# Optimization experiments

Measured on AMD Instinct MI355X. Metric: run time of the kernel, lower is better.

The kernel has to match this reference:

```python
import jax, jax.numpy as jnp
import numpy as np

B = 256          # batch
C = 1024         # d_in / d_out
S = 14           # spacial_dim
H = 8            # heads
DK = 64          # d_k
DV = 64          # d_v
N = S * S + 1    # tokens incl. mean token (197)
CONV_CH = [8, 32, 64, 128, 256, 1024]
EPS = 1e-5


def setup_inputs() -> dict:
    key = jax.random.key(0)
    ks = iter(jax.random.split(key, 32))
    d = {}
    d['feature_map'] = jax.random.normal(next(ks), (B, C, S, S), jnp.float32)
    d['loss_map'] = jax.random.normal(next(ks), (B, CONV_CH[0], S, S), jnp.float32)
    # 1x1 conv weights stored as (out_ch, in_ch)
    for i in range(5):
        cin, cout = CONV_CH[i], CONV_CH[i + 1]
        d[f'w{i+1}'] = jax.random.normal(next(ks), (cout, cin), jnp.float32) / np.sqrt(cin).astype(np.float32)
        d[f'b{i+1}'] = jnp.zeros((cout,), jnp.float32)
    # attention projections (torch Linear layout: (out, in)), xavier-ish scale
    for name, (o, i_) in [('wq', (H * DK, C)), ('wk', (H * DK, C)), ('wv', (H * DV, C)), ('wo', (C, H * DV))]:
        d[name] = jax.random.normal(next(ks), (o, i_), jnp.float32) * np.sqrt(2.0 / (o + i_)).astype(np.float32)
        d['b' + name[1]] = jnp.zeros((o,), jnp.float32)
    d['ln_g'] = jnp.ones((C,), jnp.float32)
    d['ln_b'] = jnp.zeros((C,), jnp.float32)
    d['pos_kv'] = jax.random.normal(next(ks), (N, C), jnp.float32) / np.sqrt(C).astype(np.float32)
    d['pos_q'] = jax.random.normal(next(ks), (N, C), jnp.float32) / np.sqrt(C).astype(np.float32)
    return d


def _conv1x1(x, w, b):
    # x: (b, cin, h, w); w: (cout, cin)
    return jnp.einsum('bchw,oc->bohw', x, w) + b[None, :, None, None]


def _tokens(m):
    # (b, c, h, w) -> (b, h*w, c) with prepended mean token -> (b, h*w+1, c)
    b = m.shape[0]
    t = m.reshape(b, m.shape[1], -1).transpose(0, 2, 1)
    return jnp.concatenate([t.mean(axis=1, keepdims=True), t], axis=1)


def reference(feature_map, loss_map, w1, b1, w2, b2, w3, b3, w4, b4, w5, b5,
              wq, bq, wk, bk, wv, bv, wo, bo, ln_g, ln_b, pos_kv, pos_q):
    b = feature_map.shape[0]
    # 5-stage 1x1 conv chain (pure linear, no nonlinearity)
    lm = loss_map
    for w, bi in ((w1, b1), (w2, b2), (w3, b3), (w4, b4), (w5, b5)):
        lm = _conv1x1(lm, w, bi)
    x = _tokens(feature_map) + pos_kv[None]        # (b, N, C) keys/values
    lm_t = _tokens(lm) + pos_q[None]               # (b, N, C)
    queries = lm_t[:, :1]                          # (b, 1, C) single query
    # multi-head single-query cross-attention
    q = (queries @ wq.T + bq).reshape(b, 1, H, DK).transpose(0, 2, 1, 3)   # (b,h,1,dk)
    k = (x @ wk.T + bk).reshape(b, N, H, DK).transpose(0, 2, 1, 3)         # (b,h,N,dk)
    v = (x @ wv.T + bv).reshape(b, N, H, DV).transpose(0, 2, 1, 3)         # (b,h,N,dv)
    att = jnp.einsum('bhqd,bhkd->bhqk', q, k) / jnp.asarray(np.sqrt(DK), jnp.float32)
    w_att = jax.nn.softmax(att, axis=-1)
    out = jnp.einsum('bhqk,bhkd->bhqd', w_att, v).transpose(0, 2, 1, 3).reshape(b, 1, H * DV)
    out = out @ wo.T + bo                          # (b, 1, C)
    # residual + layernorm
    res = queries + out
    mu = res.mean(axis=-1, keepdims=True)
    var = ((res - mu) ** 2).mean(axis=-1, keepdims=True)
    out = (res - mu) * jax.lax.rsqrt(var + EPS) * ln_g + ln_b
    return out.squeeze(1)                          # (b, C)
```

## Files before the change

kernel.cpp:

```cpp
#include <hip/hip_runtime.h>

#define WS_WC     ((size_t)0)
#define WS_BCQ    ((size_t)8192)
#define WS_WQP    ((size_t)9216)
#define WS_BQP    ((size_t)13312)
#define WS_U      ((size_t)13824)
#define WS_V      ((size_t)13888)
#define WS_G      ((size_t)14336)
#define WS_G0     ((size_t)79872)
#define WS_POST   ((size_t)88064)
#define WS_PSUM   ((size_t)301056)
#define WS_M0     ((size_t)302080)
#define WS_ATTP   ((size_t)304128)
#define WS_WFM    ((size_t)2008064)
#define WS_WPOS   ((size_t)2434048)
#define WS_S      ((size_t)2860032)
#define WS_OVP    ((size_t)4957184)
#define WS_O1P    ((size_t)6005760)
#define WS_POSTP  ((size_t)7054336)
#define WS_OV     ((size_t)7259136)
#define WS_M4     WS_S
#define WS_PP     WS_OVP

__global__ __launch_bounds__(256) void kp1a_chain_post(
    const float* __restrict__ w1, const float* __restrict__ b1,
    const float* __restrict__ w2, const float* __restrict__ b2,
    const float* __restrict__ w3, const float* __restrict__ b3,
    const float* __restrict__ w4, const float* __restrict__ b4,
    const float* __restrict__ pos_kv, float* __restrict__ ws)
{
  __shared__ float shm[12864];
  const int t = threadIdx.x;
  if (blockIdx.x == 0) {
    float* wt  = shm;
    float* M2s = shm + 8320;
    float* C2s = shm + 8832;
    float* M3s = shm + 8896;
    float* C3s = shm + 9920;
    float* M4s = shm + 10048;
    float* C4s = shm + 12096;

    for (int idx = t; idx < 2048; idx += 256) {
      const float4 v = ((const float4*)w3)[idx];
      const int r = idx >> 4, i = (idx & 15) * 4;
      float* d = &wt[r * 65 + i];
      d[0] = v.x; d[1] = v.y; d[2] = v.z; d[3] = v.w;
    }
    for (int idx = t; idx < 512; idx += 256) {
      const int o = idx >> 3, j = idx & 7;
      float a = 0.f;
      for (int i = 0; i < 32; ++i) a += w2[o*32+i] * w1[i*8+j];
      M2s[idx] = a;
    }
    if (t < 64) {
      float a = b2[t];
      for (int i = 0; i < 32; ++i) a += w2[t*32+i] * b1[i];
      C2s[t] = a;
    }
    __syncthreads();
    for (int idx = t; idx < 1024; idx += 256) {
      const int o = idx >> 3, j = idx & 7;
      const float* wr = &wt[o * 65];
      float a = 0.f;
      for (int i = 0; i < 64; ++i) a += wr[i] * M2s[i*8+j];
      M3s[idx] = a;
    }
    if (t < 128) {
      const float* wr = &wt[t * 65];
      float a = b3[t];
      for (int i = 0; i < 64; ++i) a += wr[i] * C2s[i];
      C3s[t] = a;
    }
    __syncthreads();
    for (int oc = 0; oc < 4; ++oc) {
      for (int idx = t; idx < 2048; idx += 256) {
        const float4 v = ((const float4*)w4)[oc*2048 + idx];
        const int r = idx >> 5, i = (idx & 31) * 4;
        float* d = &wt[r * 129 + i];
        d[0] = v.x; d[1] = v.y; d[2] = v.z; d[3] = v.w;
      }
      __syncthreads();
      for (int idx = t; idx < 512; idx += 256) {
        const int r = idx >> 3, j = idx & 7;
        const float* wr = &wt[r * 129];
        float a = 0.f;
        for (int i = 0; i < 128; ++i) a += wr[i] * M3s[i*8+j];
        M4s[(oc*64 + r)*8 + j] = a;
      }
      if (t < 64) {
        const float* wr = &wt[t * 129];
        float a = b4[oc*64 + t];
        for (int i = 0; i < 128; ++i) a += wr[i] * C3s[i];
        C4s[oc*64 + t] = a;
      }
      __syncthreads();
    }
    for (int idx = t; idx < 2048; idx += 256) ws[WS_M4 + idx] = M4s[idx];
    ws[WS_M4 + 2048 + t] = C4s[t];
  } else {
    const int c0 = (blockIdx.x - 1) * 64;
    const int c = t & 63, nb = t >> 6;
    for (int n = nb; n < 197; n += 4)
      shm[c*201 + n] = pos_kv[(size_t)n*1024 + c0 + c];
    __syncthreads();
    for (int idx = t; idx < 64*208; idx += 256) {
      int cc = idx / 208, n = idx - cc*208;
      ws[WS_POST + (size_t)(c0+cc)*208 + n] = (n < 197) ? shm[cc*201+n] : 0.f;
    }
    for (int idx = t; idx < 64*196; idx += 256) {
      int cc = idx / 196, p = idx - cc*196;
      ws[WS_POSTP + (size_t)(c0+cc)*200 + p] = shm[cc*201 + p + 1];
    }
    if (t < 64) {
      float s = 0.f;
      for (int n = 1; n < 197; ++n) s += shm[t*201 + n];
      ws[WS_PSUM + c0 + t] = s;
    }
  }
}

__global__ __launch_bounds__(256) void kp1b_w5fold(
    const float* __restrict__ w5, const float* __restrict__ b5,
    const float* __restrict__ pos_q, float* __restrict__ ws)
{
  __shared__ float wt[32 * 257];
  __shared__ float M4s[2304];
  const int t = threadIdx.x, ob = blockIdx.x;
  const int o0 = ob * 32;
  for (int idx = t; idx < 2304; idx += 256) M4s[idx] = ws[WS_M4 + idx];
  for (int idx = t; idx < 2048; idx += 256) {
    const float4 v = ((const float4*)w5)[(size_t)ob*2048 + idx];
    const int r = idx >> 6, i = (idx & 63) * 4;
    float* d = &wt[r * 257 + i];
    d[0] = v.x; d[1] = v.y; d[2] = v.z; d[3] = v.w;
  }
  __syncthreads();
  const int r = t >> 3, j = t & 7;
  const float* wr = &wt[r * 257];
  float a = 0.f;
  for (int i = 0; i < 256; ++i) a += wr[i] * M4s[i*8 + j];
  ws[WS_WC + (size_t)(o0 + r)*8 + j] = a;
  if (t < 32) {
    const float* wb = &wt[t * 257];
    float a2 = b5[o0 + t];
    for (int i = 0; i < 256; ++i) a2 += wb[i] * M4s[2048 + i];
    ws[WS_BCQ + o0 + t] = a2 + pos_q[o0 + t];
  }
}

__global__ __launch_bounds__(256) void kp2a_qproj(
    const float* __restrict__ wq, const float* __restrict__ bq,
    float* __restrict__ ws)
{
  const int t = threadIdx.x;
  const int w = t >> 6, l = t & 63;
  const int o = blockIdx.x * 4 + w;
  const float* wqr = wq + (size_t)o * 1024;
  float acc[8] = {0,0,0,0,0,0,0,0};
  float accb = 0.f;
  for (int k = 0; k < 16; ++k) {
    const int c = l + 64*k;
    const float wv_ = wqr[c];
    const float4 a  = *(const float4*)&ws[WS_WC + (size_t)c*8];
    const float4 b2 = *(const float4*)&ws[WS_WC + (size_t)c*8 + 4];
    acc[0] += wv_*a.x;  acc[1] += wv_*a.y;  acc[2] += wv_*a.z;  acc[3] += wv_*a.w;
    acc[4] += wv_*b2.x; acc[5] += wv_*b2.y; acc[6] += wv_*b2.z; acc[7] += wv_*b2.w;
    accb += wv_ * ws[WS_BCQ + c];
  }
  for (int off = 32; off >= 1; off >>= 1) {
#pragma unroll
    for (int j = 0; j < 8; ++j) acc[j] += __shfl_xor(acc[j], off);
    accb += __shfl_xor(accb, off);
  }
  if (l == 0) {
#pragma unroll
    for (int j = 0; j < 8; ++j) ws[WS_WQP + (size_t)o*8 + j] = acc[j];
    ws[WS_BQP + o] = accb + bq[o];
  }
}

__global__ __launch_bounds__(256) void kp2b_gfold(
    const float* __restrict__ wk, const float* __restrict__ bk,
    const float* __restrict__ pos_kv, float* __restrict__ ws)
{
  const int ci = blockIdx.x, h = blockIdx.y, t = threadIdx.x;
  __shared__ float WQs[512];
  __shared__ float BQs[64];
  __shared__ float red2[18 * 256];
  for (int idx = t; idx < 512; idx += 256) WQs[idx] = ws[WS_WQP + (size_t)h*512 + idx];
  if (t < 64) BQs[t] = ws[WS_BQP + h*64 + t];
  __syncthreads();

  const int c = ci*256 + t;
  float accG[8] = {0,0,0,0,0,0,0,0};
  float accg0 = 0.f;
  const float* wkc = wk + (size_t)h*64*1024 + c;
  for (int d = 0; d < 64; ++d) {
    const float wkv = wkc[(size_t)d*1024];
    const float4 qa = *(const float4*)&WQs[d*8];
    const float4 qb = *(const float4*)&WQs[d*8+4];
    accG[0] += wkv*qa.x; accG[1] += wkv*qa.y; accG[2] += wkv*qa.z; accG[3] += wkv*qa.w;
    accG[4] += wkv*qb.x; accG[5] += wkv*qb.y; accG[6] += wkv*qb.z; accG[7] += wkv*qb.w;
    accg0 += wkv * BQs[d];
  }
  *(float4*)&ws[WS_G + ((size_t)h*1024 + c)*8 + 0] = make_float4(accG[0],accG[1],accG[2],accG[3]);
  *(float4*)&ws[WS_G + ((size_t)h*1024 + c)*8 + 4] = make_float4(accG[4],accG[5],accG[6],accG[7]);
  ws[WS_G0 + (size_t)h*1024 + c] = accg0;

  const float z0 = pos_kv[c];
  const float zs = ws[WS_PSUM + c];
#pragma unroll
  for (int j = 0; j < 8; ++j) {
    red2[j*256 + t]     = accG[j]*z0;
    red2[(8+j)*256 + t] = accG[j]*zs;
  }
  red2[16*256 + t] = accg0*z0;
  red2[17*256 + t] = accg0*zs;
  __syncthreads();
  for (int s2 = 128; s2 >= 1; s2 >>= 1) {
    if (t < s2) {
#pragma unroll
      for (int j = 0; j < 18; ++j) red2[j*256 + t] += red2[j*256 + t + s2];
    }
    __syncthreads();
  }
  if (t == 0) {
    float* pp = &ws[WS_PP + ((size_t)ci*8 + h)*18];
#pragma unroll
    for (int j = 0; j < 18; ++j) pp[j] = red2[j*256];
  }

  if (ci == 0) {
    __syncthreads();
    const float bkv = (t < 64) ? bk[h*64 + t] : 0.f;
#pragma unroll
    for (int j = 0; j < 8; ++j)
      red2[j*256 + t] = (t < 64) ? bkv * WQs[t*8 + j] : 0.f;
    red2[8*256 + t] = (t < 64) ? bkv * BQs[t] : 0.f;
    __syncthreads();
    for (int s2 = 128; s2 >= 1; s2 >>= 1) {
      if (t < s2) {
#pragma unroll
        for (int j = 0; j < 9; ++j) red2[j*256 + t] += red2[j*256 + t + s2];
      }
      __syncthreads();
    }
    if (t == 0) {
#pragma unroll
      for (int j = 0; j < 8; ++j) ws[WS_U + h*8 + j] = red2[j*256];
      ws[WS_V + h] = red2[8*256];
    }
  }
}

__global__ __launch_bounds__(256) void ka_att(
    const float* __restrict__ fm, const float* __restrict__ lmap,
    float* __restrict__ ws)
{
  const int ci = blockIdx.x, b = blockIdx.y, t = threadIdx.x;
  __shared__ float qk[256 * 8];
  __shared__ float pa[3 * 49 * 33];
  __shared__ float m0s[8];
  {
    const int ch = t >> 5, lp = t & 31;
    float s = 0.f;
    for (int p = lp; p < 196; p += 32) s += lmap[((size_t)b*8 + ch)*196 + p];
    for (int off = 16; off >= 1; off >>= 1) s += __shfl_xor(s, off);
    if (lp == 0) m0s[ch] = s * (1.f/196.f);
  }
  __syncthreads();
  float m0r[8];
#pragma unroll
  for (int j = 0; j < 8; ++j) m0r[j] = m0s[j];
  const int c0 = ci * 256;
  {
    const int c = c0 + t;
#pragma unroll
    for (int h = 0; h < 8; ++h) {
      const float* gr = &ws[WS_G + ((size_t)h*1024 + c)*8];
      const float4 ga = *(const float4*)gr;
      const float4 gb = *(const float4*)(gr + 4);
      qk[t*8 + h] = ws[WS_G0 + (size_t)h*1024 + c]
                  + ga.x*m0r[0] + ga.y*m0r[1] + ga.z*m0r[2] + ga.w*m0r[3]
                  + gb.x*m0r[4] + gb.y*m0r[5] + gb.z*m0r[6] + gb.w*m0r[7];
    }
  }
  if (ci == 0 && t < 8) ws[WS_M0 + (size_t)b*8 + t] = m0s[t];
  __syncthreads();
  const int q = t >> 6, tl = t & 63;
  float a0[8] = {0,0,0,0,0,0,0,0};
  float a1[8] = {0,0,0,0,0,0,0,0};
  float a2[8] = {0,0,0,0,0,0,0,0};
  float a3[8] = {0,0,0,0,0,0,0,0};
  if (tl < 49) {
    const float* fmp = fm + ((size_t)b*1024 + c0 + q*64)*196 + 4*tl;
    const float* pp  = &ws[WS_POSTP + (size_t)(c0 + q*64)*200 + 4*tl];
    const float* qkh = &qk[q*64*8];
#pragma unroll 2
    for (int cc = 0; cc < 64; ++cc) {
      const float4 f = *(const float4*)&fmp[(size_t)cc*196];
      const float4 g = *(const float4*)&pp[(size_t)cc*200];
      const float x0 = f.x + g.x, x1 = f.y + g.y, x2 = f.z + g.z, x3 = f.w + g.w;
      const float4 qa = *(const float4*)&qkh[cc*8];
      const float4 qb = *(const float4*)&qkh[cc*8 + 4];
      a0[0] += qa.x*x0; a1[0] += qa.x*x1; a2[0] += qa.x*x2; a3[0] += qa.x*x3;
      a0[1] += qa.y*x0; a1[1] += qa.y*x1; a2[1] += qa.y*x2; a3[1] += qa.y*x3;
      a0[2] += qa.z*x0; a1[2] += qa.z*x1; a2[2] += qa.z*x2; a3[2] += qa.z*x3;
      a0[3] += qa.w*x0; a1[3] += qa.w*x1; a2[3] += qa.w*x2; a3[3] += qa.w*x3;
      a0[4] += qb.x*x0; a1[4] += qb.x*x1; a2[4] += qb.x*x2; a3[4] += qb.x*x3;
      a0[5] += qb.y*x0; a1[5] += qb.y*x1; a2[5] += qb.y*x2; a3[5] += qb.y*x3;
      a0[6] += qb.z*x0; a1[6] += qb.z*x1; a2[6] += qb.z*x2; a3[6] += qb.z*x3;
      a0[7] += qb.w*x0; a1[7] += qb.w*x1; a2[7] += qb.w*x2; a3[7] += qb.w*x3;
    }
  }
  if (q > 0 && tl < 49) {
    float* d = &pa[((q-1)*49 + tl)*33];
#pragma unroll
    for (int h = 0; h < 8; ++h) {
      d[h]    = a0[h];
      d[8+h]  = a1[h];
      d[16+h] = a2[h];
      d[24+h] = a3[h];
    }
  }
  __syncthreads();
  if (q == 0 && tl < 49) {
#pragma unroll
    for (int k = 0; k < 3; ++k) {
      const float* d = &pa[(k*49 + tl)*33];
#pragma unroll
      for (int h = 0; h < 8; ++h) {
        a0[h] += d[h];
        a1[h] += d[8+h];
        a2[h] += d[16+h];
        a3[h] += d[24+h];
      }
    }
    float* ap = &ws[WS_ATTP + (((size_t)b*4 + ci)*8)*208 + 4*tl];
#pragma unroll
    for (int h = 0; h < 8; ++h)
      *(float4*)&ap[h*208] = make_float4(a0[h], a1[h], a2[h], a3[h]);
  }
}

__global__ __launch_bounds__(256) void ksm_softmax(float* __restrict__ ws)
{
  const int b = blockIdx.x, t = threadIdx.x;
  __shared__ float red[256 * 9];
  float m0r[8];
#pragma unroll
  for (int j = 0; j < 8; ++j) m0r[j] = ws[WS_M0 + (size_t)b*8 + j];
  float qbk[8], qs0[8], qss[8];
#pragma unroll
  for (int h = 0; h < 8; ++h) {
    float s1 = ws[WS_V + h];
#pragma unroll
    for (int j = 0; j < 8; ++j) s1 += ws[WS_U + h*8 + j] * m0r[j];
    qbk[h] = s1;
    float s2 = 0.f, s3 = 0.f;
    for (int ci = 0; ci < 4; ++ci) {
      const float* pp = &ws[WS_PP + ((size_t)ci*8 + h)*18];
      float v2 = pp[16], v3 = pp[17];
#pragma unroll
      for (int j = 0; j < 8; ++j) {
        v2 += pp[j]   * m0r[j];
        v3 += pp[8+j] * m0r[j];
      }
      s2 += v2; s3 += v3;
    }
    qs0[h] = s2; qss[h] = s3;
  }
  float a[8];
#pragma unroll
  for (int h = 0; h < 8; ++h) a[h] = 0.f;
  if (t < 196) {
#pragma unroll
    for (int h = 0; h < 8; ++h) {
      float s = 0.f;
      for (int ci = 0; ci < 4; ++ci)
        s += ws[WS_ATTP + (((size_t)b*4 + ci)*8 + h)*208 + t];
      a[h] = s;
    }
  }
#pragma unroll
  for (int h = 0; h < 8; ++h) red[t*9 + h] = a[h];
  __syncthreads();
  for (int s2 = 128; s2 >= 1; s2 >>= 1) {
    if (t < s2) {
#pragma unroll
      for (int h = 0; h < 8; ++h) red[t*9+h] += red[(t+s2)*9+h];
    }
    __syncthreads();
  }
  float fa[8], fa0[8];
#pragma unroll
  for (int h = 0; h < 8; ++h) {
    const float S1 = red[h];
    fa[h]  = (a[h] + qbk[h]) * 0.125f;
    const float a0r = (S1 - qss[h]) * (1.f/196.f) + qs0[h];
    fa0[h] = (a0r + qbk[h]) * 0.125f;
  }
  __syncthreads();
#pragma unroll
  for (int h = 0; h < 8; ++h) red[t*9+h] = (t < 196) ? fa[h] : -3.0e38f;
  __syncthreads();
  for (int s2 = 128; s2 >= 1; s2 >>= 1) {
    if (t < s2) {
#pragma unroll
      for (int h = 0; h < 8; ++h) red[t*9+h] = fmaxf(red[t*9+h], red[(t+s2)*9+h]);
    }
    __syncthreads();
  }
  float mh[8];
#pragma unroll
  for (int h = 0; h < 8; ++h) mh[h] = fmaxf(red[h], fa0[h]);
  __syncthreads();
  float eh[8], e0[8];
#pragma unroll
  for (int h = 0; h < 8; ++h) {
    eh[h] = (t < 196) ? __expf(fa[h] - mh[h]) : 0.f;
    e0[h] = __expf(fa0[h] - mh[h]);
    red[t*9+h] = eh[h];
  }
  __syncthreads();
  for (int s2 = 128; s2 >= 1; s2 >>= 1) {
    if (t < s2) {
#pragma unroll
      for (int h = 0; h < 8; ++h) red[t*9+h] += red[(t+s2)*9+h];
    }
    __syncthreads();
  }
#pragma unroll
  for (int h = 0; h < 8; ++h) {
    const float lh  = red[h] + e0[h];
    const float inv = 1.f / lh;
    const float w0  = e0[h] * inv;
    float* wfm = &ws[WS_WFM  + ((size_t)b*8 + h)*208];
    float* wpo = &ws[WS_WPOS + ((size_t)b*8 + h)*208];
    if (t < 196) {
      wfm[t]   = eh[h]*inv + w0*(1.f/196.f);
      wpo[t+1] = eh[h]*inv;
    } else if (t < 208) {
      wfm[t] = 0.f;
      if (t == 196) wpo[0] = w0;
      else          wpo[t] = 0.f;
    }
  }
}

__global__ __launch_bounds__(256) void kb_fm(
    const float* __restrict__ fm, float* __restrict__ ws)
{
  __shared__ float fms[64 * 224];
  __shared__ float wfs[1664];
  const int cj = blockIdx.x, b = blockIdx.y, t = threadIdx.x;
  const int c0 = cj * 64;
  const float4* src = (const float4*)(fm + ((size_t)b*1024 + c0)*196);
  for (int r = 0; r < 3; ++r) {
    float4 v[4];
#pragma unroll
    for (int u = 0; u < 4; ++u) v[u] = src[t + (r*4 + u)*256];
#pragma unroll
    for (int u = 0; u < 4; ++u) {
      const int idx = t + (r*4 + u)*256;
      const int c = idx / 49, qq = idx - c*49;
      *(float4*)&fms[c*224 + ((qq ^ (c & 7)) << 2)] = v[u];
    }
  }
  if (t < 64) {
    const int idx = t + 3072;
    const float4 v = src[idx];
    const int c = idx / 49, qq = idx - c*49;
    *(float4*)&fms[c*224 + ((qq ^ (c & 7)) << 2)] = v;
  }
  {
    const float4* wsrc = (const float4*)&ws[WS_WFM + (size_t)b*1664];
    float4 w0 = wsrc[t & 255];
    float4 w1 = (t < 160) ? wsrc[256 + t] : make_float4(0,0,0,0);
    *(float4*)&wfs[(t & 255)*4] = w0;
    if (t < 160) *(float4*)&wfs[(256 + t)*4] = w1;
  }
  __syncthreads();
  const int c = t & 63, hh = t >> 6;
  const int h0 = hh*2, h1 = h0+1;
  const int cx = (c & 7) << 2;
  const float* fr = &fms[c*224];
  const float* w0p = &wfs[h0*208];
  const float* w1p = &wfs[h1*208];
  float a0 = 0.f, a1 = 0.f;
#pragma unroll 7
  for (int p4 = 0; p4 < 49; ++p4) {
    const float4 f  = *(const float4*)&fr[((p4 << 2) ^ cx)];
    const float4 u0 = *(const float4*)&w0p[p4*4];
    const float4 u1 = *(const float4*)&w1p[p4*4];
    a0 += f.x*u0.x + f.y*u0.y + f.z*u0.z + f.w*u0.w;
    a1 += f.x*u1.x + f.y*u1.y + f.z*u1.z + f.w*u1.w;
  }
  ws[WS_S + ((size_t)h0*256 + b)*1024 + c0 + c] = a0;
  ws[WS_S + ((size_t)h1*256 + b)*1024 + c0 + c] = a1;
}

__global__ __launch_bounds__(256) void kb_pos(float* __restrict__ ws)
{
  __shared__ float As[64 * 108];
  __shared__ float Bs[64 * 108];
  const int ct = blockIdx.x, rt = blockIdx.y, t = threadIdx.x;
  const int c0 = ct*64, r0 = rt*64;
  const int bq = t >> 4, cq = t & 15;
  float acc[4][4] = {};
  for (int sub = 0; sub < 2; ++sub) {
    const int k0 = sub * 104;
    __syncthreads();
    for (int idx = t; idx < 1664; idx += 256) {
      const int r = idx / 26, q = idx - r*26;
      const float4 av = *(const float4*)&ws[WS_WPOS + (size_t)(r0 + r)*208 + k0 + q*4];
      float* da = &As[r*108 + q*4];
      da[0]=av.x; da[1]=av.y; da[2]=av.z; da[3]=av.w;
      const float4 bv = *(const float4*)&ws[WS_POST + (size_t)(c0 + r)*208 + k0 + q*4];
      float* db = &Bs[r*108 + q*4];
      db[0]=bv.x; db[1]=bv.y; db[2]=bv.z; db[3]=bv.w;
    }
    __syncthreads();
    for (int k4 = 0; k4 < 26; ++k4) {
      float4 av[4], bw[4];
#pragma unroll
      for (int i = 0; i < 4; ++i) av[i] = *(const float4*)&As[(bq + 16*i)*108 + k4*4];
#pragma unroll
      for (int j = 0; j < 4; ++j) bw[j] = *(const float4*)&Bs[(cq + 16*j)*108 + k4*4];
#pragma unroll
      for (int i = 0; i < 4; ++i)
#pragma unroll
        for (int j = 0; j < 4; ++j)
          acc[i][j] += av[i].x*bw[j].x + av[i].y*bw[j].y + av[i].z*bw[j].z + av[i].w*bw[j].w;
    }
  }
#pragma unroll
  for (int i = 0; i < 4; ++i) {
    const int rIdx = r0 + bq + 16*i;
    const int b = rIdx >> 3, h = rIdx & 7;
    float* srow = &ws[WS_S + ((size_t)h*256 + b)*1024];
#pragma unroll
    for (int j = 0; j < 4; ++j) {
      const int c = c0 + cq + 16*j;
      srow[c] += acc[i][j];
    }
  }
}

__global__ __launch_bounds__(256) void kv_ov(
    const float* __restrict__ wv, float* __restrict__ ws)
{
  const int kt = blockIdx.x, bt = blockIdx.y, h = blockIdx.z, t = threadIdx.x;
  __shared__ float At[64 * 65];
  __shared__ float Bt[64 * 65];
  const int b0 = bt*64, k0 = kt*128;
  const int bq = t >> 4, dq = t & 15;
  float acc[4][4] = {};
  for (int sub = 0; sub < 2; ++sub) {
    const int kk0 = k0 + sub*64;
    __syncthreads();
    for (int r = 0; r < 4; ++r) {
      const int idx = t + 256*r;
      const int bi = idx >> 4, c4 = idx & 15;
      const float4 v = *(const float4*)&ws[WS_S + ((size_t)h*256 + b0 + bi)*1024 + kk0 + c4*4];
      float* d1 = &At[bi*65 + c4*4];
      d1[0]=v.x; d1[1]=v.y; d1[2]=v.z; d1[3]=v.w;
      const float4 w = *(const float4*)&wv[(size_t)(h*64 + bi)*1024 + kk0 + c4*4];
      float* d2 = &Bt[bi*65 + c4*4];
      d2[0]=w.x; d2[1]=w.y; d2[2]=w.z; d2[3]=w.w;
    }
    __syncthreads();
    for (int kk = 0; kk < 64; ++kk) {
      float av[4], bw[4];
#pragma unroll
      for (int i = 0; i < 4; ++i) av[i] = At[(bq*4+i)*65 + kk];
#pragma unroll
      for (int j = 0; j < 4; ++j) bw[j] = Bt[(dq*4+j)*65 + kk];
#pragma unroll
      for (int i = 0; i < 4; ++i)
#pragma unroll
        for (int j = 0; j < 4; ++j) acc[i][j] += av[i]*bw[j];
    }
  }
#pragma unroll
  for (int i = 0; i < 4; ++i) {
    *(float4*)&ws[WS_OVP + ((size_t)kt*256 + b0 + bq*4 + i)*512 + h*64 + dq*4] =
        make_float4(acc[i][0], acc[i][1], acc[i][2], acc[i][3]);
  }
}

__global__ __launch_bounds__(256) void kor_ovred(
    const float* __restrict__ bv, float* __restrict__ ws)
{
  const int b = blockIdx.x, t = threadIdx.x;
  for (int j = t; j < 512; j += 256) {
    float s = bv[j];
    for (int kt = 0; kt < 8; ++kt)
      s += ws[WS_OVP + ((size_t)kt*256 + b)*512 + j];
    ws[WS_OV + (size_t)b*512 + j] = s;
  }
}

__global__ __launch_bounds__(256) void ko_out(
    const float* __restrict__ wo, float* __restrict__ ws)
{
  const int kt2 = blockIdx.x, ct = blockIdx.y, bt = blockIdx.z, t = threadIdx.x;
  __shared__ float At[64 * 65];
  __shared__ float Bt[64 * 65];
  const int b0 = bt*64, c0 = ct*64, j0 = kt2*128;
  const int bq = t >> 4, cq = t & 15;
  float acc[4][4] = {};
  for (int sub = 0; sub < 2; ++sub) {
    const int jj0 = j0 + sub*64;
    __syncthreads();
    for (int r = 0; r < 4; ++r) {
      const int idx = t + 256*r;
      const int bi = idx >> 4, j4 = idx & 15;
      const float4 p = *(const float4*)&ws[WS_OV + (size_t)(b0 + bi)*512 + jj0 + j4*4];
      float* d1 = &At[bi*65 + j4*4];
      d1[0]=p.x; d1[1]=p.y; d1[2]=p.z; d1[3]=p.w;
      const float4 w = *(const float4*)&wo[(size_t)(c0 + bi)*512 + jj0 + j4*4];
      float* d2 = &Bt[bi*65 + j4*4];
      d2[0]=w.x; d2[1]=w.y; d2[2]=w.z; d2[3]=w.w;
    }
    __syncthreads();
    for (int jj = 0; jj < 64; ++jj) {
      float av[4], bw[4];
#pragma unroll
      for (int i = 0; i < 4; ++i) av[i] = At[(bq*4+i)*65 + jj];
#pragma unroll
      for (int j = 0; j < 4; ++j) bw[j] = Bt[(cq*4+j)*65 + jj];
#pragma unroll
      for (int i = 0; i < 4; ++i)
#pragma unroll
        for (int j = 0; j < 4; ++j) acc[i][j] += av[i]*bw[j];
    }
  }
#pragma unroll
  for (int i = 0; i < 4; ++i) {
    *(float4*)&ws[WS_O1P + ((size_t)kt2*256 + b0 + bq*4 + i)*1024 + c0 + cq*4] =
        make_float4(acc[i][0], acc[i][1], acc[i][2], acc[i][3]);
  }
}

__global__ __launch_bounds__(256) void kln_final(
    const float* __restrict__ bo, const float* __restrict__ ln_g,
    const float* __restrict__ ln_b, const float* __restrict__ ws,
    float* __restrict__ out)
{
  const int b = blockIdx.x, t = threadIdx.x;
  __shared__ float rs[256], rq[256];
  float m0r[8];
#pragma unroll
  for (int j = 0; j < 8; ++j) m0r[j] = ws[WS_M0 + (size_t)b*8 + j];
  float r[4];
  float sum = 0.f, sumsq = 0.f;
  for (int k = 0; k < 4; ++k) {
    const int c = t + 256*k;
    float o1 = bo[c];
    for (int kt2 = 0; kt2 < 4; ++kt2)
      o1 += ws[WS_O1P + ((size_t)kt2*256 + b)*1024 + c];
    const float* wc = &ws[WS_WC + c*8];
    float qv = ws[WS_BCQ + c];
#pragma unroll
    for (int j = 0; j < 8; ++j) qv += wc[j]*m0r[j];
    const float res = qv + o1;
    r[k] = res; sum += res; sumsq += res*res;
  }
  rs[t] = sum; rq[t] = sumsq;
  __syncthreads();
  for (int s2 = 128; s2 >= 1; s2 >>= 1) {
    if (t < s2) { rs[t] += rs[t+s2]; rq[t] += rq[t+s2]; }
    __syncthreads();
  }
  const float mu  = rs[0] * (1.f/1024.f);
  const float var = rq[0] * (1.f/1024.f) - mu*mu;
  const float inv = rsqrtf(var + 1e-5f);
  for (int k = 0; k < 4; ++k) {
    const int c = t + 256*k;
    out[(size_t)b*1024 + c] = (r[k] - mu)*inv*ln_g[c] + ln_b[c];
  }
}

extern "C" void kernel_launch(void* const* d_in, const int* in_sizes, int n_in,
                              void* d_out, int out_size, void* d_ws, size_t ws_size,
                              hipStream_t stream)
{
  const float* fm   = (const float*)d_in[0];
  const float* lmap = (const float*)d_in[1];
  const float* w1 = (const float*)d_in[2];  const float* b1 = (const float*)d_in[3];
  const float* w2 = (const float*)d_in[4];  const float* b2 = (const float*)d_in[5];
  const float* w3 = (const float*)d_in[6];  const float* b3 = (const float*)d_in[7];
  const float* w4 = (const float*)d_in[8];  const float* b4 = (const float*)d_in[9];
  const float* w5 = (const float*)d_in[10]; const float* b5 = (const float*)d_in[11];
  const float* wq = (const float*)d_in[12]; const float* bq = (const float*)d_in[13];
  const float* wk = (const float*)d_in[14]; const float* bk = (const float*)d_in[15];
  const float* wv = (const float*)d_in[16]; const float* bv = (const float*)d_in[17];
  const float* wo = (const float*)d_in[18]; const float* bo = (const float*)d_in[19];
  const float* ln_g = (const float*)d_in[20]; const float* ln_b = (const float*)d_in[21];
  const float* pos_kv = (const float*)d_in[22]; const float* pos_q = (const float*)d_in[23];
  float* ws  = (float*)d_ws;
  float* out = (float*)d_out;

  kp1a_chain_post<<<dim3(17), dim3(256), 0, stream>>>(w1,b1,w2,b2,w3,b3,w4,b4,pos_kv,ws);
  kp1b_w5fold<<<dim3(32), dim3(256), 0, stream>>>(w5,b5,pos_q,ws);
  kp2a_qproj<<<dim3(128), dim3(256), 0, stream>>>(wq,bq,ws);
  kp2b_gfold<<<dim3(4,8), dim3(256), 0, stream>>>(wk,bk,pos_kv,ws);
  ka_att<<<dim3(4,256), dim3(256), 0, stream>>>(fm,lmap,ws);
  ksm_softmax<<<dim3(256), dim3(256), 0, stream>>>(ws);
  kb_fm<<<dim3(16,256), dim3(256), 0, stream>>>(fm,ws);
  kb_pos<<<dim3(16,32), dim3(256), 0, stream>>>(ws);
  kv_ov<<<dim3(8,4,8), dim3(256), 0, stream>>>(wv,ws);
  kor_ovred<<<dim3(256), dim3(256), 0, stream>>>(bv,ws);
  ko_out<<<dim3(4,16,4), dim3(256), 0, stream>>>(wo,ws);
  kln_final<<<dim3(256), dim3(256), 0, stream>>>(bo,ln_g,ln_b,ws,out);
}
```

Before: 222.8 us.

## Fold positional-key contribution into precomputed per-head tables; use wave-shuffle softmax reductions

The positional term of the attention logits is split out by linearity. A new kernel precomputes, per head and per token, the projection of pos_kv onto the folded query-key matrices. The softmax kernel then rebuilds that part from the batch's mean loss-map vector. This removes the pos_kv stream from the hot attention loop, which now reads only the feature map. The softmax kernel also replaces shared-memory tree reductions with wavefront shuffles plus a small cross-wave combine. The cost is one more launch and each softmax block loading and summing a ~60 KB table into LDS, which may lower occupancy.

After: 239.8 us. +7.6%, slower.

```diff
diff --git a/kernel.cpp b/kernel.cpp
--- a/kernel.cpp
+++ b/kernel.cpp
@@ -17,7 +17,7 @@
 #define WS_S      ((size_t)2860032)
 #define WS_OVP    ((size_t)4957184)
 #define WS_O1P    ((size_t)6005760)
-#define WS_POSTP  ((size_t)7054336)
+#define WS_AJP    ((size_t)7054336)
 #define WS_OV     ((size_t)7259136)
 #define WS_M4     WS_S
 #define WS_PP     WS_OVP
@@ -107,10 +107,6 @@
       int cc = idx / 208, n = idx - cc*208;
       ws[WS_POST + (size_t)(c0+cc)*208 + n] = (n < 197) ? shm[cc*201+n] : 0.f;
     }
-    for (int idx = t; idx < 64*196; idx += 256) {
-      int cc = idx / 196, p = idx - cc*196;
-      ws[WS_POSTP + (size_t)(c0+cc)*200 + p] = shm[cc*201 + p + 1];
-    }
     if (t < 64) {
       float s = 0.f;
       for (int n = 1; n < 197; ++n) s += shm[t*201 + n];
@@ -253,6 +249,37 @@
   }
 }
 
+__global__ __launch_bounds__(256) void kaj_pfold(float* __restrict__ ws)
+{
+  __shared__ float Gs[256 * 12];
+  const int blk = blockIdx.x, t = threadIdx.x;
+  const int ci = blk & 3, h = blk >> 2;
+  const int c0 = ci * 256;
+  for (int idx = t; idx < 2048; idx += 256) {
+    const int c = idx >> 3, j = idx & 7;
+    Gs[c*12 + j] = ws[WS_G + ((size_t)h*1024 + c0 + c)*8 + j];
+  }
+  Gs[t*12 + 8] = ws[WS_G0 + (size_t)h*1024 + c0 + t];
+  __syncthreads();
+  float acc[9] = {0,0,0,0,0,0,0,0,0};
+  if (t < 196) {
+    for (int cc = 0; cc < 256; ++cc) {
+      const float z = ws[WS_POST + (size_t)(c0 + cc)*208 + t + 1];
+      const float4 ga = *(const float4*)&Gs[cc*12];
+      const float4 gb = *(const float4*)&Gs[cc*12 + 4];
+      const float  gc = Gs[cc*12 + 8];
+      acc[0] += ga.x*z; acc[1] += ga.y*z; acc[2] += ga.z*z; acc[3] += ga.w*z;
+      acc[4] += gb.x*z; acc[5] += gb.y*z; acc[6] += gb.z*z; acc[7] += gb.w*z;
+      acc[8] += gc*z;
+    }
+  }
+  if (t < 208) {
+    float* dst = &ws[WS_AJP + (size_t)(ci*8 + h)*9*208];
+#pragma unroll
+    for (int j = 0; j < 9; ++j) dst[j*208 + t] = (t < 196) ? acc[j] : 0.f;
+  }
+}
+
 __global__ __launch_bounds__(256) void ka_att(
     const float* __restrict__ fm, const float* __restrict__ lmap,
     float* __restrict__ ws)
@@ -294,23 +321,20 @@
   float a3[8] = {0,0,0,0,0,0,0,0};
   if (tl < 49) {
     const float* fmp = fm + ((size_t)b*1024 + c0 + q*64)*196 + 4*tl;
-    const float* pp  = &ws[WS_POSTP + (size_t)(c0 + q*64)*200 + 4*tl];
     const float* qkh = &qk[q*64*8];
 #pragma unroll 2
     for (int cc = 0; cc < 64; ++cc) {
       const float4 f = *(const float4*)&fmp[(size_t)cc*196];
-      const float4 g = *(const float4*)&pp[(size_t)cc*200];
-      const float x0 = f.x + g.x, x1 = f.y + g.y, x2 = f.z + g.z, x3 = f.w + g.w;
       const float4 qa = *(const float4*)&qkh[cc*8];
       const float4 qb = *(const float4*)&qkh[cc*8 + 4];
-      a0[0] += qa.x*x0; a1[0] += qa.x*x1; a2[0] += qa.x*x2; a3[0] += qa.x*x3;
-      a0[1] += qa.y*x0; a1[1] += qa.y*x1; a2[1] += qa.y*x2; a3[1] += qa.y*x3;
-      a0[2] += qa.z*x0; a1[2] += qa.z*x1; a2[2] += qa.z*x2; a3[2] += qa.z*x3;
-      a0[3] += qa.w*x0; a1[3] += qa.w*x1; a2[3] += qa.w*x2; a3[3] += qa.w*x3;
-      a0[4] += qb.x*x0; a1[4] += qb.x*x1; a2[4] += qb.x*x2; a3[4] += qb.x*x3;
-      a0[5] += qb.y*x0; a1[5] += qb.y*x1; a2[5] += qb.y*x2; a3[5] += qb.y*x3;
-      a0[6] += qb.z*x0; a1[6] += qb.z*x1; a2[6] += qb.z*x2; a3[6] += qb.z*x3;
-      a0[7] += qb.w*x0; a1[7] += qb.w*x1; a2[7] += qb.w*x2; a3[7] += qb.w*x3;
+      a0[0] += qa.x*f.x; a1[0] += qa.x*f.y; a2[0] += qa.x*f.z; a3[0] += qa.x*f.w;
+      a0[1] += qa.y*f.x; a1[1] += qa.y*f.y; a2[1] += qa.y*f.z; a3[1] += qa.y*f.w;
+      a0[2] += qa.z*f.x; a1[2] += qa.z*f.y; a2[2] += qa.z*f.z; a3[2] += qa.z*f.w;
+      a0[3] += qa.w*f.x; a1[3] += qa.w*f.y; a2[3] += qa.w*f.z; a3[3] += qa.w*f.w;
+      a0[4] += qb.x*f.x; a1[4] += qb.x*f.y; a2[4] += qb.x*f.z; a3[4] += qb.x*f.w;
+      a0[5] += qb.y*f.x; a1[5] += qb.y*f.y; a2[5] += qb.y*f.z; a3[5] += qb.y*f.w;
+      a0[6] += qb.z*f.x; a1[6] += qb.z*f.y; a2[6] += qb.z*f.z; a3[6] += qb.z*f.w;
+      a0[7] += qb.w*f.x; a1[7] += qb.w*f.y; a2[7] += qb.w*f.z; a3[7] += qb.w*f.w;
     }
   }
   if (q > 0 && tl < 49) {
@@ -345,34 +369,42 @@
 
 __global__ __launch_bounds__(256) void ksm_softmax(float* __restrict__ ws)
 {
+  __shared__ float AJs[8 * 9 * 208];
+  __shared__ float wredA[32], wredB[32], wredC[32];
   const int b = blockIdx.x, t = threadIdx.x;
-  __shared__ float red[256 * 9];
+  const int wv_ = t >> 6;
+  {
+    const float4* p0 = (const float4*)&ws[WS_AJP + 0*14976];
+    const float4* p1 = (const float4*)&ws[WS_AJP + 1*14976];
+    const float4* p2 = (const float4*)&ws[WS_AJP + 2*14976];
+    const float4* p3 = (const float4*)&ws[WS_AJP + 3*14976];
+    for (int idx = t; idx < 3744; idx += 256) {
+      const float4 v0 = p0[idx], v1 = p1[idx], v2 = p2[idx], v3 = p3[idx];
+      *(float4*)&AJs[idx*4] = make_float4(v0.x+v1.x+v2.x+v3.x, v0.y+v1.y+v2.y+v3.y,
+                                          v0.z+v1.z+v2.z+v3.z, v0.w+v1.w+v2.w+v3.w);
+    }
+  }
   float m0r[8];
 #pragma unroll
   for (int j = 0; j < 8; ++j) m0r[j] = ws[WS_M0 + (size_t)b*8 + j];
-  float qbk[8], qs0[8], qss[8];
+  float qbk[8], qs0[8];
 #pragma unroll
   for (int h = 0; h < 8; ++h) {
     float s1 = ws[WS_V + h];
 #pragma unroll
     for (int j = 0; j < 8; ++j) s1 += ws[WS_U + h*8 + j] * m0r[j];
     qbk[h] = s1;
-    float s2 = 0.f, s3 = 0.f;
+    float s2 = 0.f;
     for (int ci = 0; ci < 4; ++ci) {
       const float* pp = &ws[WS_PP + ((size_t)ci*8 + h)*18];
-      float v2 = pp[16], v3 = pp[17];
-#pragma unroll
-      for (int j = 0; j < 8; ++j) {
-        v2 += pp[j]   * m0r[j];
-        v3 += pp[8+j] * m0r[j];
-      }
-      s2 += v2; s3 += v3;
-    }
-    qs0[h] = s2; qss[h] = s3;
-  }
-  float a[8];
-#pragma unroll
-  for (int h = 0; h < 8; ++h) a[h] = 0.f;
+      float v2 = pp[16];
+#pragma unroll
+      for (int j = 0; j < 8; ++j) v2 += pp[j] * m0r[j];
+      s2 += v2;
+    }
+    qs0[h] = s2;
+  }
+  float a[8] = {0,0,0,0,0,0,0,0};
   if (t < 196) {
 #pragma unroll
     for (int h = 0; h < 8; ++h) {
@@ -382,57 +414,79 @@
       a[h] = s;
     }
   }
-#pragma unroll
-  for (int h = 0; h < 8; ++h) red[t*9 + h] = a[h];
-  __syncthreads();
-  for (int s2 = 128; s2 >= 1; s2 >>= 1) {
-    if (t < s2) {
-#pragma unroll
-      for (int h = 0; h < 8; ++h) red[t*9+h] += red[(t+s2)*9+h];
-    }
-    __syncthreads();
+  {
+    float r[8];
+#pragma unroll
+    for (int h = 0; h < 8; ++h) r[h] = a[h];
+    for (int off = 32; off >= 1; off >>= 1) {
+#pragma unroll
+      for (int h = 0; h < 8; ++h) r[h] += __shfl_xor(r[h], off);
+    }
+    if ((t & 63) == 0) {
+#pragma unroll
+      for (int h = 0; h < 8; ++h) wredA[wv_*8 + h] = r[h];
+    }
+  }
+  __syncthreads();
+  float pa[8] = {0,0,0,0,0,0,0,0};
+  if (t < 196) {
+#pragma unroll
+    for (int h = 0; h < 8; ++h) {
+      const float* aj = &AJs[h*9*208];
+      float v = aj[8*208 + t];
+#pragma unroll
+      for (int j = 0; j < 8; ++j) v += aj[j*208 + t] * m0r[j];
+      pa[h] = v;
+    }
   }
   float fa[8], fa0[8];
 #pragma unroll
   for (int h = 0; h < 8; ++h) {
-    const float S1 = red[h];
-    fa[h]  = (a[h] + qbk[h]) * 0.125f;
-    const float a0r = (S1 - qss[h]) * (1.f/196.f) + qs0[h];
-    fa0[h] = (a0r + qbk[h]) * 0.125f;
-  }
-  __syncthreads();
-#pragma unroll
-  for (int h = 0; h < 8; ++h) red[t*9+h] = (t < 196) ? fa[h] : -3.0e38f;
-  __syncthreads();
-  for (int s2 = 128; s2 >= 1; s2 >>= 1) {
-    if (t < s2) {
-#pragma unroll
-      for (int h = 0; h < 8; ++h) red[t*9+h] = fmaxf(red[t*9+h], red[(t+s2)*9+h]);
-    }
-    __syncthreads();
-  }
+    const float S1 = wredA[h] + wredA[8+h] + wredA[16+h] + wredA[24+h];
+    fa[h]  = (a[h] + pa[h] + qbk[h]) * 0.125f;
+    fa0[h] = (S1*(1.f/196.f) + qs0[h] + qbk[h]) * 0.125f;
+  }
+  {
+    float r[8];
+#pragma unroll
+    for (int h = 0; h < 8; ++h) r[h] = (t < 196) ? fa[h] : -3.0e38f;
+    for (int off = 32; off >= 1; off >>= 1) {
+#pragma unroll
+      for (int h = 0; h < 8; ++h) r[h] = fmaxf(r[h], __shfl_xor(r[h], off));
+    }
+    if ((t & 63) == 0) {
+#pragma unroll
+      for (int h = 0; h < 8; ++h) wredB[wv_*8 + h] = r[h];
+    }
+  }
+  __syncthreads();
   float mh[8];
 #pragma unroll
-  for (int h = 0; h < 8; ++h) mh[h] = fmaxf(red[h], fa0[h]);
-  __syncthreads();
+  for (int h = 0; h < 8; ++h)
+    mh[h] = fmaxf(fmaxf(fmaxf(wredB[h], wredB[8+h]), fmaxf(wredB[16+h], wredB[24+h])), fa0[h]);
   float eh[8], e0[8];
 #pragma unroll
   for (int h = 0; h < 8; ++h) {
     eh[h] = (t < 196) ? __expf(fa[h] - mh[h]) : 0.f;
     e0[h] = __expf(fa0[h] - mh[h]);
-    red[t*9+h] = eh[h];
-  }
-  __syncthreads();
-  for (int s2 = 128; s2 >= 1; s2 >>= 1) {
-    if (t < s2) {
-#pragma unroll
-      for (int h = 0; h < 8; ++h) red[t*9+h] += red[(t+s2)*9+h];
-    }
-    __syncthreads();
-  }
+  }
+  {
+    float r[8];
+#pragma unroll
+    for (int h = 0; h < 8; ++h) r[h] = eh[h];
+    for (int off = 32; off >= 1; off >>= 1) {
+#pragma unroll
+      for (int h = 0; h < 8; ++h) r[h] += __shfl_xor(r[h], off);
+    }
+    if ((t & 63) == 0) {
+#pragma unroll
+      for (int h = 0; h < 8; ++h) wredC[wv_*8 + h] = r[h];
+    }
+  }
+  __syncthreads();
 #pragma unroll
   for (int h = 0; h < 8; ++h) {
-    const float lh  = red[h] + e0[h];
+    const float lh  = wredC[h] + wredC[8+h] + wredC[16+h] + wredC[24+h] + e0[h];
     const float inv = 1.f / lh;
     const float w0  = e0[h] * inv;
     float* wfm = &ws[WS_WFM  + ((size_t)b*8 + h)*208];
@@ -706,6 +760,7 @@
   kp1b_w5fold<<<dim3(32), dim3(256), 0, stream>>>(w5,b5,pos_q,ws);
   kp2a_qproj<<<dim3(128), dim3(256), 0, stream>>>(wq,bq,ws);
   kp2b_gfold<<<dim3(4,8), dim3(256), 0, stream>>>(wk,bk,pos_kv,ws);
+  kaj_pfold<<<dim3(32), dim3(256), 0, stream>>>(ws);
   ka_att<<<dim3(4,256), dim3(256), 0, stream>>>(fm,lmap,ws);
   ksm_softmax<<<dim3(256), dim3(256), 0, stream>>>(ws);
   kb_fm<<<dim3(16,256), dim3(256), 0, stream>>>(fm,ws);
```
